# Kernel tuning notes

Measured on AMD Instinct MI355X. Metric: run time of the kernel, lower is better.

The kernel has to match this reference:

```python
import jax, jax.numpy as jnp
import numpy as np

N_WIRES = 4
N_LAYERS = 3
B = 65536
EPS = 1e-5


def setup_inputs() -> dict:
    key = jax.random.key(0)
    ks = jax.random.split(key, 8)
    return {
        "x": jax.random.normal(ks[0], (B, 1, 28, 28), jnp.float32),
        "pre_fc_w": jax.random.normal(ks[1], (N_WIRES, 16), jnp.float32) * 0.25,
        "pre_fc_b": jax.random.normal(ks[2], (N_WIRES,), jnp.float32) * 0.25,
        "weights": jax.random.normal(ks[3], (N_LAYERS, N_WIRES, 2), jnp.float32),
        "fc_w": jax.random.normal(ks[4], (4, N_WIRES), jnp.float32) * 0.5,
        "fc_b": jax.random.normal(ks[5], (4,), jnp.float32) * 0.5,
        "bn_gamma": jnp.ones((4,), jnp.float32),
        "bn_beta": jnp.zeros((4,), jnp.float32),
    }


def _rx_mat(theta):
    # RX(t) = [[cos t/2, -i sin t/2], [-i sin t/2, cos t/2]]; theta scalar or [B]
    half = theta * 0.5
    c = jnp.cos(half).astype(jnp.complex64)
    s = (-1j) * jnp.sin(half).astype(jnp.complex64)
    return jnp.stack([jnp.stack([c, s], -1), jnp.stack([s, c], -1)], -2)


def _rz_mat(theta):
    # RZ(t) = diag(e^{-it/2}, e^{it/2})
    half = theta * 0.5
    e = jnp.exp((-1j) * half.astype(jnp.complex64))
    z = jnp.zeros_like(e)
    return jnp.stack([jnp.stack([e, z], -1), jnp.stack([z, jnp.conj(e)], -1)], -2)


def _apply_1q(state, mat, wire):
    # state: [B,2,2,2,2]; mat: [2,2] or [B,2,2]
    s = jnp.moveaxis(state, wire + 1, -1)
    if mat.ndim == 3:
        s = jnp.einsum('bij,b...j->b...i', mat, s)
    else:
        s = jnp.einsum('ij,b...j->b...i', mat, s)
    return jnp.moveaxis(s, -1, wire + 1)


def _cnot(state, c, t):
    s = jnp.moveaxis(state, (c + 1, t + 1), (-2, -1))
    s = jnp.stack([s[..., 0, :], s[..., 1, ::-1]], axis=-2)
    return jnp.moveaxis(s, (-2, -1), (c + 1, t + 1))


def _circuit(encoded, weights):
    # encoded: [B, n_wires] angles; returns per-wire <Z> expvals [B, n_wires]
    b = encoded.shape[0]
    state = jnp.zeros((b,) + (2,) * N_WIRES, jnp.complex64).at[:, 0, 0, 0, 0].set(1.0)
    for w in range(N_WIRES):
        state = _apply_1q(state, _rx_mat(encoded[:, w]), w)
    for l in range(N_LAYERS):
        for w in range(N_WIRES):
            state = _apply_1q(state, _rx_mat(weights[l, w, 0]), w)
            state = _apply_1q(state, _rz_mat(weights[l, w, 1]), w)
        for w in range(N_WIRES):
            state = _cnot(state, w, (w + 1) % N_WIRES)
    probs = jnp.abs(state) ** 2  # [B,2,2,2,2] float32
    zvals = []
    for w in range(N_WIRES):
        shape = [1] + [2 if i == w else 1 for i in range(N_WIRES)]
        sign = jnp.array([1.0, -1.0], jnp.float32).reshape(shape)
        zvals.append(jnp.sum(probs * sign, axis=tuple(range(1, N_WIRES + 1))))
    return jnp.stack(zvals, -1)


def reference(x, pre_fc_w, pre_fc_b, weights, fc_w, fc_b, bn_gamma, bn_beta):
    bsz = x.shape[0]
    # avg_pool2d kernel=6 stride=6 (valid): windows cover the first 24x24 pixels -> 4x4
    pooled = x[:, :, :24, :24].reshape(bsz, 1, 4, 6, 4, 6).mean(axis=(3, 5)).reshape(bsz, 16)
    encoded = pooled @ pre_fc_w.T + pre_fc_b          # [B, n_wires]
    q_out = _circuit(encoded, weights)                # [B, n_wires]
    logits = q_out @ fc_w.T + fc_b                    # [B, 4]
    mean = logits.mean(axis=0)
    var = logits.var(axis=0)                          # biased var (training-mode BN)
    return (logits - mean) / jnp.sqrt(var + EPS) * bn_gamma + bn_beta
```

## Files before the change

### kernel.cpp

```cpp
#include <hip/hip_runtime.h>
#include <math.h>

#define NB 65536
#define NBLK1 1024
#define IMGS1 64

__global__ __launch_bounds__(256) void fused_kernel(
        const float* __restrict__ x,
        const float* __restrict__ pre_w,
        const float* __restrict__ pre_b,
        const float* __restrict__ weights,
        const float* __restrict__ fc_w,
        const float* __restrict__ fc_b,
        float4* __restrict__ out,
        float* __restrict__ partial) {
    __shared__ float2 Wl[256];
    __shared__ float4 enc[IMGS1];
    const int tid = threadIdx.x;

    if (tid >= 192 && tid < 208) {
        const int t = tid - 192;
        float cr[16], ci[16];
#pragma unroll
        for (int i = 0; i < 16; ++i) { cr[i] = (i == t) ? 1.0f : 0.0f; ci[i] = 0.0f; }

        for (int l = 0; l < 3; ++l) {
#pragma unroll
            for (int w = 0; w < 4; ++w) {
                const int mask = 8 >> w;
                float tx = weights[(l * 4 + w) * 2 + 0] * 0.5f;
                float c = cosf(tx), s = sinf(tx);
#pragma unroll
                for (int i = 0; i < 16; ++i) {
                    if (!(i & mask)) {
                        const int ip = i | mask;
                        float a0r = cr[i], a0i = ci[i], a1r = cr[ip], a1i = ci[ip];
                        cr[i]  = c * a0r + s * a1i;
                        ci[i]  = c * a0i - s * a1r;
                        cr[ip] = c * a1r + s * a0i;
                        ci[ip] = c * a1i - s * a0r;
                    }
                }
                float tz = weights[(l * 4 + w) * 2 + 1] * 0.5f;
                float ce = cosf(tz), se = sinf(tz);
#pragma unroll
                for (int i = 0; i < 16; ++i) {
                    if (!(i & mask)) {
                        const int ip = i | mask;
                        float a0r = cr[i], a0i = ci[i], a1r = cr[ip], a1i = ci[ip];
                        cr[i]  = ce * a0r + se * a0i;
                        ci[i]  = ce * a0i - se * a0r;
                        cr[ip] = ce * a1r - se * a1i;
                        ci[ip] = ce * a1i + se * a1r;
                    }
                }
            }
#pragma unroll
            for (int w = 0; w < 4; ++w) {
                const int mc = 8 >> w;
                const int mt = 8 >> ((w + 1) & 3);
#pragma unroll
                for (int i = 0; i < 16; ++i) {
                    if ((i & mc) && !(i & mt)) {
                        const int ip = i | mt;
                        float tr = cr[i], ti = ci[i];
                        cr[i] = cr[ip]; ci[i] = ci[ip];
                        cr[ip] = tr;   ci[ip] = ti;
                    }
                }
            }
        }
        int p = __popc(t) & 3;
#pragma unroll
        for (int i = 0; i < 16; ++i) {
            float wr, wi;
            if (p == 0)      { wr =  cr[i]; wi =  ci[i]; }
            else if (p == 1) { wr =  ci[i]; wi = -cr[i]; }
            else if (p == 2) { wr = -cr[i]; wi = -ci[i]; }
            else             { wr = -ci[i]; wi =  cr[i]; }
            Wl[i * 16 + t] = make_float2(wr, wi);
        }
    }

    const int h1 = tid & 3;
    const size_t img_idx = (size_t)blockIdx.x * IMGS1 + (tid >> 2);
    const float* img = x + img_idx * 784 + (size_t)h1 * 168;

    float cs0 = 0.f, cs1 = 0.f, cs2 = 0.f, cs3 = 0.f;
#pragma unroll
    for (int r = 0; r < 6; ++r) {
        const float4* row = (const float4*)(img + r * 28);
        float4 f0 = row[0], f1 = row[1], f2 = row[2];
        float4 f3 = row[3], f4 = row[4], f5 = row[5];
        cs0 += f0.x + f0.y + f0.z + f0.w + f1.x + f1.y;
        cs1 += f1.z + f1.w + f2.x + f2.y + f2.z + f2.w;
        cs2 += f3.x + f3.y + f3.z + f3.w + f4.x + f4.y;
        cs3 += f4.z + f4.w + f5.x + f5.y + f5.z + f5.w;
    }
    const float inv36 = 1.0f / 36.0f;
    cs0 *= inv36; cs1 *= inv36; cs2 *= inv36; cs3 *= inv36;

    const int k0 = h1 * 4;
    float p0 = cs0 * pre_w[k0]      + cs1 * pre_w[k0 + 1] +
               cs2 * pre_w[k0 + 2]  + cs3 * pre_w[k0 + 3];
    float p1 = cs0 * pre_w[16 + k0] + cs1 * pre_w[16 + k0 + 1] +
               cs2 * pre_w[16 + k0 + 2] + cs3 * pre_w[16 + k0 + 3];
    float p2 = cs0 * pre_w[32 + k0] + cs1 * pre_w[32 + k0 + 1] +
               cs2 * pre_w[32 + k0 + 2] + cs3 * pre_w[32 + k0 + 3];
    float p3 = cs0 * pre_w[48 + k0] + cs1 * pre_w[48 + k0 + 1] +
               cs2 * pre_w[48 + k0 + 2] + cs3 * pre_w[48 + k0 + 3];

    p0 += __shfl_xor(p0, 1); p0 += __shfl_xor(p0, 2);
    p1 += __shfl_xor(p1, 1); p1 += __shfl_xor(p1, 2);
    p2 += __shfl_xor(p2, 1); p2 += __shfl_xor(p2, 2);
    p3 += __shfl_xor(p3, 1); p3 += __shfl_xor(p3, 2);

    if (h1 == 0) {
        enc[tid >> 2] = make_float4(p0 + pre_b[0], p1 + pre_b[1],
                                    p2 + pre_b[2], p3 + pre_b[3]);
    }
    __syncthreads();

    if (tid < IMGS1) {
        float4 e = enc[tid];
        float s0, c0, s1, c1, s2, c2, s3, c3;
        __sincosf(e.x * 0.5f, &s0, &c0);
        __sincosf(e.y * 0.5f, &s1, &c1);
        __sincosf(e.z * 0.5f, &s2, &c2);
        __sincosf(e.w * 0.5f, &s3, &c3);

        float m01[4] = { c0 * c1, c0 * s1, s0 * c1, s0 * s1 };
        float m23[4] = { c2 * c3, c2 * s3, s2 * c3, s2 * s3 };
        float m[16];
#pragma unroll
        for (int i = 0; i < 16; ++i) m[i] = m01[i >> 2] * m23[i & 3];

        float z0 = 0.f, z1 = 0.f, z2 = 0.f, z3 = 0.f;
#pragma unroll
        for (int i = 0; i < 16; ++i) {
            float sr = 0.f, si = 0.f;
#pragma unroll
            for (int j = 0; j < 16; ++j) {
                float2 w = Wl[i * 16 + j];
                sr += w.x * m[j];
                si += w.y * m[j];
            }
            float pr = sr * sr + si * si;
            z0 += (i & 8) ? -pr : pr;
            z1 += (i & 4) ? -pr : pr;
            z2 += (i & 2) ? -pr : pr;
            z3 += (i & 1) ? -pr : pr;
        }

        float l0 = fc_b[0] + fc_w[0]  * z0 + fc_w[1]  * z1 + fc_w[2]  * z2 + fc_w[3]  * z3;
        float l1 = fc_b[1] + fc_w[4]  * z0 + fc_w[5]  * z1 + fc_w[6]  * z2 + fc_w[7]  * z3;
        float l2 = fc_b[2] + fc_w[8]  * z0 + fc_w[9]  * z1 + fc_w[10] * z2 + fc_w[11] * z3;
        float l3 = fc_b[3] + fc_w[12] * z0 + fc_w[13] * z1 + fc_w[14] * z2 + fc_w[15] * z3;
        out[(size_t)blockIdx.x * IMGS1 + tid] = make_float4(l0, l1, l2, l3);

        float s[8] = { l0, l1, l2, l3, l0 * l0, l1 * l1, l2 * l2, l3 * l3 };
#pragma unroll
        for (int off = 32; off; off >>= 1) {
#pragma unroll
            for (int q = 0; q < 8; ++q) s[q] += __shfl_down(s[q], off);
        }
        if (tid == 0) {
            float4* p = (float4*)(partial + (size_t)blockIdx.x * 8);
            p[0] = make_float4(s[0], s[1], s[2], s[3]);
            p[1] = make_float4(s[4], s[5], s[6], s[7]);
        }
    }
}

__global__ __launch_bounds__(256) void finalize_kernel(
        float4* __restrict__ out,
        const float* __restrict__ partial,
        const float* __restrict__ gamma,
        const float* __restrict__ beta) {
    __shared__ float red4[4][8];
    __shared__ float scsh[8];
    const int tid = threadIdx.x;

    float s[8];
#pragma unroll
    for (int q = 0; q < 8; ++q) s[q] = 0.f;
#pragma unroll
    for (int r = 0; r < NBLK1 / 256; ++r) {
        const float4* row = (const float4*)(partial + (size_t)(tid + r * 256) * 8);
        float4 a = row[0], c = row[1];
        s[0] += a.x; s[1] += a.y; s[2] += a.z; s[3] += a.w;
        s[4] += c.x; s[5] += c.y; s[6] += c.z; s[7] += c.w;
    }
#pragma unroll
    for (int off = 32; off; off >>= 1) {
#pragma unroll
        for (int q = 0; q < 8; ++q) s[q] += __shfl_down(s[q], off);
    }
    if ((tid & 63) == 0) {
#pragma unroll
        for (int q = 0; q < 8; ++q) red4[tid >> 6][q] = s[q];
    }
    __syncthreads();
    if (tid < 8) {
        red4[0][tid] = red4[0][tid] + red4[1][tid] + red4[2][tid] + red4[3][tid];
    }
    __syncthreads();
    if (tid < 4) {
        const float invB = 1.0f / (float)NB;
        float mean = red4[0][tid] * invB;
        float var  = red4[0][4 + tid] * invB - mean * mean;
        float inv  = rsqrtf(var + 1e-5f);
        float g = gamma[tid];
        scsh[tid]     = g * inv;
        scsh[4 + tid] = beta[tid] - mean * g * inv;
    }
    __syncthreads();

    const float sc0 = scsh[0], sc1 = scsh[1], sc2 = scsh[2], sc3 = scsh[3];
    const float sh0 = scsh[4], sh1 = scsh[5], sh2 = scsh[6], sh3 = scsh[7];
    const int b = blockIdx.x * 256 + tid;
    float4 v = out[b];
    v.x = v.x * sc0 + sh0;
    v.y = v.y * sc1 + sh1;
    v.z = v.z * sc2 + sh2;
    v.w = v.w * sc3 + sh3;
    out[b] = v;
}

extern "C" void kernel_launch(void* const* d_in, const int* in_sizes, int n_in,
                              void* d_out, int out_size, void* d_ws, size_t ws_size,
                              hipStream_t stream) {
    const float* x       = (const float*)d_in[0];
    const float* pre_w   = (const float*)d_in[1];
    const float* pre_b   = (const float*)d_in[2];
    const float* weights = (const float*)d_in[3];
    const float* fc_w    = (const float*)d_in[4];
    const float* fc_b    = (const float*)d_in[5];
    const float* gamma   = (const float*)d_in[6];
    const float* beta    = (const float*)d_in[7];

    float* partial = (float*)d_ws;

    hipLaunchKernelGGL(fused_kernel, dim3(NBLK1), dim3(256), 0, stream,
                       x, pre_w, pre_b, weights, fc_w, fc_b,
                       (float4*)d_out, partial);
    hipLaunchKernelGGL(finalize_kernel, dim3(NB / 256), dim3(256), 0, stream,
                       (float4*)d_out, partial, gamma, beta);
}
```

Measured before the change: 44.13 us.

## Stream image block with coalesced float4 loads and LDS atomic pooling

The pooling stage now has all 256 threads read the block's 64 images as one contiguous float4 stream, instead of each thread reading strided rows from a single image. Each thread maps its element to an image, row band and column window and accumulates into a shared-memory accumulator with atomicAdd. It also reads the rows and columns the pooling discards (rows 24-27 and the 7th float4 of each row), since the whole block is now loaded. The intent is fully coalesced global loads to get closer to bandwidth, at the cost of about 14% more bytes loaded, LDS atomic contention, integer div/mod per element, and an extra zeroing pass with a barrier.

```diff
diff --git a/kernel.cpp b/kernel.cpp
--- a/kernel.cpp
+++ b/kernel.cpp
@@ -4,6 +4,10 @@
 #define NB 65536
 #define NBLK1 1024
 #define IMGS1 64
+#define F4_PER_IMG 196
+#define F4_PER_BLK (IMGS1 * F4_PER_IMG)
+#define ITERS (F4_PER_BLK / 256)
+#define ACC_STRIDE 17
 
 __global__ __launch_bounds__(256) void fused_kernel(
         const float* __restrict__ x,
@@ -15,8 +19,15 @@
         float4* __restrict__ out,
         float* __restrict__ partial) {
     __shared__ float2 Wl[256];
-    __shared__ float4 enc[IMGS1];
+    __shared__ float acc[IMGS1][ACC_STRIDE];
     const int tid = threadIdx.x;
+
+#pragma unroll
+    for (int i = 0; i < (IMGS1 * ACC_STRIDE + 255) / 256; ++i) {
+        int idx = i * 256 + tid;
+        if (idx < IMGS1 * ACC_STRIDE) ((float*)acc)[idx] = 0.f;
+    }
+    __syncthreads();
 
     if (tid >= 192 && tid < 208) {
         const int t = tid - 192;
@@ -82,52 +93,43 @@
         }
     }
 
-    const int h1 = tid & 3;
-    const size_t img_idx = (size_t)blockIdx.x * IMGS1 + (tid >> 2);
-    const float* img = x + img_idx * 784 + (size_t)h1 * 168;
-
-    float cs0 = 0.f, cs1 = 0.f, cs2 = 0.f, cs3 = 0.f;
-#pragma unroll
-    for (int r = 0; r < 6; ++r) {
-        const float4* row = (const float4*)(img + r * 28);
-        float4 f0 = row[0], f1 = row[1], f2 = row[2];
-        float4 f3 = row[3], f4 = row[4], f5 = row[5];
-        cs0 += f0.x + f0.y + f0.z + f0.w + f1.x + f1.y;
-        cs1 += f1.z + f1.w + f2.x + f2.y + f2.z + f2.w;
-        cs2 += f3.x + f3.y + f3.z + f3.w + f4.x + f4.y;
-        cs3 += f4.z + f4.w + f5.x + f5.y + f5.z + f5.w;
-    }
-    const float inv36 = 1.0f / 36.0f;
-    cs0 *= inv36; cs1 *= inv36; cs2 *= inv36; cs3 *= inv36;
-
-    const int k0 = h1 * 4;
-    float p0 = cs0 * pre_w[k0]      + cs1 * pre_w[k0 + 1] +
-               cs2 * pre_w[k0 + 2]  + cs3 * pre_w[k0 + 3];
-    float p1 = cs0 * pre_w[16 + k0] + cs1 * pre_w[16 + k0 + 1] +
-               cs2 * pre_w[16 + k0 + 2] + cs3 * pre_w[16 + k0 + 3];
-    float p2 = cs0 * pre_w[32 + k0] + cs1 * pre_w[32 + k0 + 1] +
-               cs2 * pre_w[32 + k0 + 2] + cs3 * pre_w[32 + k0 + 3];
-    float p3 = cs0 * pre_w[48 + k0] + cs1 * pre_w[48 + k0 + 1] +
-               cs2 * pre_w[48 + k0 + 2] + cs3 * pre_w[48 + k0 + 3];
-
-    p0 += __shfl_xor(p0, 1); p0 += __shfl_xor(p0, 2);
-    p1 += __shfl_xor(p1, 1); p1 += __shfl_xor(p1, 2);
-    p2 += __shfl_xor(p2, 1); p2 += __shfl_xor(p2, 2);
-    p3 += __shfl_xor(p3, 1); p3 += __shfl_xor(p3, 2);
-
-    if (h1 == 0) {
-        enc[tid >> 2] = make_float4(p0 + pre_b[0], p1 + pre_b[1],
-                                    p2 + pre_b[2], p3 + pre_b[3]);
+    const float4* xin = (const float4*)x + (size_t)blockIdx.x * F4_PER_BLK;
+#pragma unroll 7
+    for (int k = 0; k < ITERS; ++k) {
+        const int idx = k * 256 + tid;
+        float4 v = xin[idx];
+        const int img = idx / F4_PER_IMG;
+        const int rem = idx - img * F4_PER_IMG;
+        const int row = rem / 7;
+        const int q   = rem - row * 7;
+        if (row < 24 && q < 6) {
+            const int band = row / 6;
+            float* a = &acc[img][band * 4];
+            const int lo = (q * 4) / 6;
+            const int hi = (q * 4 + 3) / 6;
+            atomicAdd(&a[lo], v.x + v.y);
+            atomicAdd(&a[hi], v.z + v.w);
+        }
     }
     __syncthreads();
 
     if (tid < IMGS1) {
-        float4 e = enc[tid];
+        const float inv36 = 1.0f / 36.0f;
+        float e0 = pre_b[0], e1 = pre_b[1], e2 = pre_b[2], e3 = pre_b[3];
+#pragma unroll
+        for (int k = 0; k < 16; ++k) {
+            float a = acc[tid][k] * inv36;
+            e0 += a * pre_w[k];
+            e1 += a * pre_w[16 + k];
+            e2 += a * pre_w[32 + k];
+            e3 += a * pre_w[48 + k];
+        }
+
         float s0, c0, s1, c1, s2, c2, s3, c3;
-        __sincosf(e.x * 0.5f, &s0, &c0);
-        __sincosf(e.y * 0.5f, &s1, &c1);
-        __sincosf(e.z * 0.5f, &s2, &c2);
-        __sincosf(e.w * 0.5f, &s3, &c3);
+        __sincosf(e0 * 0.5f, &s0, &c0);
+        __sincosf(e1 * 0.5f, &s1, &c1);
+        __sincosf(e2 * 0.5f, &s2, &c2);
+        __sincosf(e3 * 0.5f, &s3, &c3);
 
         float m01[4] = { c0 * c1, c0 * s1, s0 * c1, s0 * s1 };
         float m23[4] = { c2 * c3, c2 * s3, s2 * c3, s2 * s3 };
@@ -162,7 +164,7 @@
 #pragma unroll
         for (int off = 32; off; off >>= 1) {
 #pragma unroll
-            for (int q = 0; q < 8; ++q) s[q] += __shfl_down(s[q], off);
+            for (int q2 = 0; q2 < 8; ++q2) s[q2] += __shfl_down(s[q2], off);
         }
         if (tid == 0) {
             float4* p = (float4*)(partial + (size_t)blockIdx.x * 8);
```

New measurement: 123.0 us. +178.7%, slower.
